# Kernel tuning notes

Measured on AMD Instinct MI355X. Metric: run time of the kernel, lower is better.

Reference implementation:

```python
import jax
import jax.numpy as jnp
from jax import lax
import numpy as np


def design_butter_hp_sos(order: int, cutoff: float, fs: float) -> np.ndarray:
    """Pure-numpy replica of scipy.signal.butter(order, cutoff, 'hp', fs=fs, output='sos')."""
    Wn = cutoff / (fs / 2.0)          # normalized to Nyquist
    fs_b = 2.0                        # scipy's internal sampling rate convention
    warped = 2.0 * fs_b * np.tan(np.pi * Wn / fs_b)  # prewarped analog cutoff
    # Analog Butterworth lowpass prototype poles (buttap)
    m = np.arange(-order + 1, order, 2)
    p_lp = -np.exp(1j * np.pi * m / (2 * order))
    k = np.real(np.prod(-p_lp))       # == 1 for Butterworth
    # lp2hp: zeros at s=0, poles -> warped / p
    p_hp = warped / p_lp
    z_hp = np.zeros(order, dtype=complex)
    # bilinear transform (fs2 = 2 * fs_b)
    fs2 = 2.0 * fs_b
    p_z = (fs2 + p_hp) / (fs2 - p_hp)
    k_z = k * np.real(np.prod(fs2 - z_hp) / np.prod(fs2 - p_hp))
    # pair conjugate poles into biquads; scipy puts poles nearest unit circle LAST
    pos = p_z[np.imag(p_z) > 0]
    pos = pos[np.argsort(np.abs(pos))]
    n_sec = order // 2
    sos = np.zeros((n_sec, 6))
    for i, p in enumerate(pos):
        b = np.array([1.0, -2.0, 1.0])  # two zeros at z = 1 (DC block)
        if i == 0:
            b = b * k_z                 # overall gain lives in the first section
        sos[i, :3] = b
        sos[i, 3:] = np.array([1.0, -2.0 * p.real, np.abs(p) ** 2])
    return sos.astype(np.float32)


def setup_inputs() -> dict:
    key = jax.random.key(0)
    audio = jax.random.normal(key, (64, 480000), dtype=jnp.float32)  # [batch, samples]
    sos = jnp.asarray(design_butter_hp_sos(4, 80.0, 16000.0))        # [2, 6]
    return {"audio": audio, "sos": sos}


def _sosfilt(sos, x):
    """Cascade biquad IIR (direct form II transposed), zero initial state.
    x: [B, T], sos: [n_sections, 6]. Batch is vectorized inside the scan carry."""
    B = x.shape[0]

    def one_section(x, coefs):
        b0, b1, b2, _, a1, a2 = coefs

        def step(state, xn):
            s0, s1 = state                 # each [B]
            y = b0 * xn + s0
            s0_new = b1 * xn - a1 * y + s1
            s1_new = b2 * xn - a2 * y
            return (s0_new, s1_new), y

        init = (jnp.zeros(B, x.dtype), jnp.zeros(B, x.dtype))
        _, y = lax.scan(step, init, x.T)   # scan over time, [T, B]
        return y.T

    for i in range(sos.shape[0]):          # small static loop over 2 sections
        x = one_section(x, sos[i])
    return x


def reference(audio, sos):
    squeeze = audio.ndim == 1
    x = audio[None, :] if squeeze else audio
    y = _sosfilt(sos, x)
    return y[0] if squeeze else y
```

## Files before the change

### kernel.cpp

```cpp
#include <hip/hip_runtime.h>


#define SEG   32
#define F4S   (SEG / 4)
#define NT    32
#define SEGS  256
#define EMITS (SEGS - NT)

typedef float f32x4 __attribute__((ext_vector_type(4)));

struct Coefs { float b00,b01,b02,a01,a02,b10,b11,b12,a11,a12; };

__device__ __forceinline__ void step(const Coefs& c, float xn,
    float& s10, float& s11, float& s20, float& s21, float& yout) {
  float y1 = fmaf(c.b00, xn, s10);
  s10 = fmaf(-c.a01, y1, fmaf(c.b01, xn, s11));
  s11 = fmaf(-c.a02, y1, c.b02 * xn);
  float y2 = fmaf(c.b10, y1, s20);
  s20 = fmaf(-c.a11, y2, fmaf(c.b11, y1, s21));
  s21 = fmaf(-c.a12, y2, c.b12 * y1);
  yout = y2;
}

__device__ __forceinline__ Coefs load_coefs(const float* __restrict__ sos) {
  Coefs c;
  c.b00=sos[0]; c.b01=sos[1]; c.b02=sos[2]; c.a01=sos[4];  c.a02=sos[5];
  c.b10=sos[6]; c.b11=sos[7]; c.b12=sos[8]; c.a11=sos[10]; c.a12=sos[11];
  return c;
}

__global__ __launch_bounds__(256, 4) void iir_fused(
    const float* __restrict__ x, const float* __restrict__ sos,
    float* __restrict__ out, int T, int nchunks, int bpr) {
  __shared__ f32x4 stg[SEGS * F4S];
  __shared__ f32x4 u[SEGS];

  int row = blockIdx.x / bpr;
  int blk = blockIdx.x - row * bpr;
  int k = threadIdx.x;
  int sbase = blk * EMITS - NT;
  int myseg = sbase + k;
  int perm = k & 7;
  Coefs c = load_coefs(sos);

  const f32x4* xr4 = reinterpret_cast<const f32x4*>(x) + (size_t)row * (T >> 2);
  f32x4*       yr4 = reinterpret_cast<f32x4*>(out)     + (size_t)row * (T >> 2);
  const f32x4 z4 = {0.f, 0.f, 0.f, 0.f};

  f32x4 t0,t1,t2,t3,t4,t5,t6,t7;
#define PREF(IT, TR) { int f_ = k + IT*256; int s_ = f_>>3; int gs_ = sbase + s_; \
    TR = (gs_ >= 0 && gs_ < nchunks) ? xr4[(size_t)gs_ * F4S + (f_&7)] : z4; }
#define WST(IT, TR) { int f_ = k + IT*256; int s_ = f_>>3, j_ = f_&7; \
    stg[s_*F4S + (j_^(s_&7))] = TR; }
  PREF(0,t0) PREF(1,t1) PREF(2,t2) PREF(3,t3)
  PREF(4,t4) PREF(5,t5) PREF(6,t6) PREF(7,t7)
  WST(0,t0) WST(1,t1) WST(2,t2) WST(3,t3)
  WST(4,t4) WST(5,t5) WST(6,t6) WST(7,t7)
  __syncthreads();

  {
    float s10 = 0.f, s11 = 0.f, s20 = 0.f, s21 = 0.f, d_;
#pragma unroll
    for (int j = 0; j < F4S; ++j) {
      f32x4 v = stg[k * F4S + (j ^ perm)];
      step(c, v[0], s10, s11, s20, s21, d_);
      step(c, v[1], s10, s11, s20, s21, d_);
      step(c, v[2], s10, s11, s20, s21, d_);
      step(c, v[3], s10, s11, s20, s21, d_);
    }
    f32x4 uu; uu[0] = s10; uu[1] = s11; uu[2] = s20; uu[3] = s21;
    u[k] = uu;
  }
  __syncthreads();

  float P[16];
  {
    float A[16];
#pragma unroll
    for (int col = 0; col < 4; ++col) {
      float a0 = (col == 0), a1 = (col == 1), a2 = (col == 2), a3 = (col == 3), dd;
      step(c, 0.f, a0, a1, a2, a3, dd);
      A[0 * 4 + col] = a0; A[1 * 4 + col] = a1;
      A[2 * 4 + col] = a2; A[3 * 4 + col] = a3;
    }
#pragma unroll
    for (int i = 0; i < 16; ++i) P[i] = A[i];
#pragma unroll
    for (int it = 0; it < 5; ++it) {
      float Q[16];
#pragma unroll
      for (int r = 0; r < 4; ++r)
#pragma unroll
        for (int cc = 0; cc < 4; ++cc) {
          float acc = 0.f;
#pragma unroll
          for (int kk = 0; kk < 4; ++kk) acc = fmaf(P[r * 4 + kk], P[kk * 4 + cc], acc);
          Q[r * 4 + cc] = acc;
        }
#pragma unroll
      for (int i = 0; i < 16; ++i) P[i] = Q[i];
    }
  }

  bool emits = (k >= NT) && (myseg < nchunks);
  if (emits) {
    float h0 = 0.f, h1 = 0.f, h2 = 0.f, h3 = 0.f;
#pragma unroll
    for (int kk = NT; kk >= 1; --kk) {
      f32x4 uu = u[k - kk];
      float q0 = fmaf(P[0],  h0, fmaf(P[1],  h1, fmaf(P[2],  h2, P[3]  * h3)));
      float q1 = fmaf(P[4],  h0, fmaf(P[5],  h1, fmaf(P[6],  h2, P[7]  * h3)));
      float q2 = fmaf(P[8],  h0, fmaf(P[9],  h1, fmaf(P[10], h2, P[11] * h3)));
      float q3 = fmaf(P[12], h0, fmaf(P[13], h1, fmaf(P[14], h2, P[15] * h3)));
      h0 = uu[0] + q0; h1 = uu[1] + q1; h2 = uu[2] + q2; h3 = uu[3] + q3;
    }
    float s10 = h0, s11 = h1, s20 = h2, s21 = h3;
#pragma unroll
    for (int j = 0; j < F4S; ++j) {
      f32x4 v = stg[k * F4S + (j ^ perm)];
      f32x4 yv; float yo;
      step(c, v[0], s10, s11, s20, s21, yo); yv[0] = yo;
      step(c, v[1], s10, s11, s20, s21, yo); yv[1] = yo;
      step(c, v[2], s10, s11, s20, s21, yo); yv[2] = yo;
      step(c, v[3], s10, s11, s20, s21, yo); yv[3] = yo;
      stg[k * F4S + (j ^ perm)] = yv;
    }
  }
  __syncthreads();

  int eseg0 = blk * EMITS;
  int nemit = nchunks - eseg0; if (nemit > EMITS) nemit = EMITS;
  if (nemit > 0) {
    int F = nemit * F4S;
    f32x4* dst = yr4 + (size_t)eseg0 * F4S;
    for (int f = k; f < F; f += 256) {
      int s = f >> 3, j = f & 7;
      int ls = s + NT;
      dst[f] = stg[ls * F4S + (j ^ (ls & 7))];
    }
  }
}

#define FB_C 256
#define FB_W 1024
__global__ __launch_bounds__(256) void sosfilt2_chunked(
    const float* __restrict__ x, const float* __restrict__ sos,
    float* __restrict__ out, int B, int T, int nchunks) {
  int tid = blockIdx.x * 256 + threadIdx.x;
  if (tid >= B * nchunks) return;
  int row = tid / nchunks;
  int chunk = tid - row * nchunks;
  Coefs c = load_coefs(sos);
  const float* xr = x + (size_t)row * T;
  float*       yr = out + (size_t)row * T;
  int c0   = chunk * FB_C;
  int cend = min(c0 + FB_C, T);
  int warm = min(FB_W, c0);
  int t    = c0 - warm;
  float s10 = 0.f, s11 = 0.f, s20 = 0.f, s21 = 0.f;
  float dump;
  for (; t < c0; t += 4) {
    f32x4 xvv = *reinterpret_cast<const f32x4*>(xr + t);
#pragma unroll
    for (int j = 0; j < 4; ++j) step(c, xvv[j], s10, s11, s20, s21, dump);
  }
  int tv_end = c0 + ((cend - c0) & ~3);
  for (; t < tv_end; t += 4) {
    f32x4 xvv = *reinterpret_cast<const f32x4*>(xr + t);
    f32x4 yv;
#pragma unroll
    for (int j = 0; j < 4; ++j) {
      float yo;
      step(c, xvv[j], s10, s11, s20, s21, yo);
      yv[j] = yo;
    }
    *reinterpret_cast<f32x4*>(yr + t) = yv;
  }
  for (; t < cend; ++t) { float yv; step(c, xr[t], s10, s11, s20, s21, yv); yr[t] = yv; }
}

extern "C" void kernel_launch(void* const* d_in, const int* in_sizes, int n_in,
                              void* d_out, int out_size, void* d_ws, size_t ws_size,
                              hipStream_t stream) {
  const float* x   = (const float*)d_in[0];
  const float* sos = (const float*)d_in[1];
  float*       out = (float*)d_out;

  int total = in_sizes[0];
  int T = 480000;
  if (total % T != 0) T = total;
  int B = total / T;

  if (T % SEG == 0) {
    int nchunks = T / SEG;
    int bpr = (nchunks + EMITS - 1) / EMITS;
    iir_fused<<<B * bpr, 256, 0, stream>>>(x, sos, out, T, nchunks, bpr);
  } else {
    int nc = (T + FB_C - 1) / FB_C;
    int grid = (B * nc + 255) / 256;
    sosfilt2_chunked<<<grid, 256, 0, stream>>>(x, sos, out, B, T, nc);
  }
}
```

Measured before the change: 50.18 us.

## Replace serial 32-step state propagation with log-depth parallel scan using precomputed matrix powers

```diff
diff --git a/kernel.cpp b/kernel.cpp
--- a/kernel.cpp
+++ b/kernel.cpp
@@ -29,11 +29,49 @@
   return c;
 }
 
+__global__ void iir_setup(const float* __restrict__ sos, float* __restrict__ ws) {
+  if (blockIdx.x != 0 || threadIdx.x != 0) return;
+  Coefs c = load_coefs(sos);
+  float P[16];
+  {
+    float A[16];
+    for (int col = 0; col < 4; ++col) {
+      float a0 = (col == 0), a1 = (col == 1), a2 = (col == 2), a3 = (col == 3), dd;
+      step(c, 0.f, a0, a1, a2, a3, dd);
+      A[0*4+col] = a0; A[1*4+col] = a1; A[2*4+col] = a2; A[3*4+col] = a3;
+    }
+    for (int i = 0; i < 16; ++i) P[i] = A[i];
+    for (int it = 0; it < 5; ++it) {
+      float Q[16];
+      for (int r = 0; r < 4; ++r)
+        for (int cc = 0; cc < 4; ++cc) {
+          float acc = 0.f;
+          for (int kk = 0; kk < 4; ++kk) acc = fmaf(P[r*4+kk], P[kk*4+cc], acc);
+          Q[r*4+cc] = acc;
+        }
+      for (int i = 0; i < 16; ++i) P[i] = Q[i];
+    }
+  }
+  for (int l = 0; l < 5; ++l) {
+    for (int i = 0; i < 16; ++i) ws[l*16 + i] = P[i];
+    float Q[16];
+    for (int r = 0; r < 4; ++r)
+      for (int cc = 0; cc < 4; ++cc) {
+        float acc = 0.f;
+        for (int kk = 0; kk < 4; ++kk) acc = fmaf(P[r*4+kk], P[kk*4+cc], acc);
+        Q[r*4+cc] = acc;
+      }
+    for (int i = 0; i < 16; ++i) P[i] = Q[i];
+  }
+}
+
 __global__ __launch_bounds__(256, 4) void iir_fused(
     const float* __restrict__ x, const float* __restrict__ sos,
-    float* __restrict__ out, int T, int nchunks, int bpr) {
+    const float* __restrict__ ws, float* __restrict__ out,
+    int T, int nchunks, int bpr) {
   __shared__ f32x4 stg[SEGS * F4S];
-  __shared__ f32x4 u[SEGS];
+  __shared__ f32x4 va[SEGS];
+  __shared__ f32x4 vb[SEGS];
 
   int row = blockIdx.x / bpr;
   int blk = blockIdx.x - row * bpr;
@@ -69,52 +107,48 @@
       step(c, v[3], s10, s11, s20, s21, d_);
     }
     f32x4 uu; uu[0] = s10; uu[1] = s11; uu[2] = s20; uu[3] = s21;
-    u[k] = uu;
-  }
-  __syncthreads();
-
-  float P[16];
-  {
-    float A[16];
-#pragma unroll
-    for (int col = 0; col < 4; ++col) {
-      float a0 = (col == 0), a1 = (col == 1), a2 = (col == 2), a3 = (col == 3), dd;
-      step(c, 0.f, a0, a1, a2, a3, dd);
-      A[0 * 4 + col] = a0; A[1 * 4 + col] = a1;
-      A[2 * 4 + col] = a2; A[3 * 4 + col] = a3;
-    }
-#pragma unroll
-    for (int i = 0; i < 16; ++i) P[i] = A[i];
-#pragma unroll
-    for (int it = 0; it < 5; ++it) {
-      float Q[16];
-#pragma unroll
-      for (int r = 0; r < 4; ++r)
-#pragma unroll
-        for (int cc = 0; cc < 4; ++cc) {
-          float acc = 0.f;
-#pragma unroll
-          for (int kk = 0; kk < 4; ++kk) acc = fmaf(P[r * 4 + kk], P[kk * 4 + cc], acc);
-          Q[r * 4 + cc] = acc;
-        }
-#pragma unroll
-      for (int i = 0; i < 16; ++i) P[i] = Q[i];
-    }
-  }
+    va[k] = uu;
+  }
+  __syncthreads();
+
+  {
+    f32x4 vprev = (k >= 1) ? va[k - 1] : z4;
+    __syncthreads();
+    va[k] = vprev;
+  }
+  __syncthreads();
+
+  {
+    f32x4* src = va;
+    f32x4* dst = vb;
+#pragma unroll
+    for (int l = 0; l < 5; ++l) {
+      float p0  = ws[l*16+0],  p1  = ws[l*16+1],  p2  = ws[l*16+2],  p3  = ws[l*16+3];
+      float p4  = ws[l*16+4],  p5  = ws[l*16+5],  p6  = ws[l*16+6],  p7  = ws[l*16+7];
+      float p8  = ws[l*16+8],  p9  = ws[l*16+9],  p10 = ws[l*16+10], p11 = ws[l*16+11];
+      float p12 = ws[l*16+12], p13 = ws[l*16+13], p14 = ws[l*16+14], p15 = ws[l*16+15];
+      f32x4 mine = src[k];
+      int off = 1 << l;
+      f32x4 r = mine;
+      if (k >= off) {
+        f32x4 w = src[k - off];
+        r[0] = mine[0] + fmaf(p0,  w[0], fmaf(p1,  w[1], fmaf(p2,  w[2], p3  * w[3])));
+        r[1] = mine[1] + fmaf(p4,  w[0], fmaf(p5,  w[1], fmaf(p6,  w[2], p7  * w[3])));
+        r[2] = mine[2] + fmaf(p8,  w[0], fmaf(p9,  w[1], fmaf(p10, w[2], p11 * w[3])));
+        r[3] = mine[3] + fmaf(p12, w[0], fmaf(p13, w[1], fmaf(p14, w[2], p15 * w[3])));
+      }
+      dst[k] = r;
+      __syncthreads();
+      f32x4* tmp = src; src = dst; dst = tmp;
+    }
+    va[k] = src[k];
+  }
+  __syncthreads();
 
   bool emits = (k >= NT) && (myseg < nchunks);
   if (emits) {
-    float h0 = 0.f, h1 = 0.f, h2 = 0.f, h3 = 0.f;
-#pragma unroll
-    for (int kk = NT; kk >= 1; --kk) {
-      f32x4 uu = u[k - kk];
-      float q0 = fmaf(P[0],  h0, fmaf(P[1],  h1, fmaf(P[2],  h2, P[3]  * h3)));
-      float q1 = fmaf(P[4],  h0, fmaf(P[5],  h1, fmaf(P[6],  h2, P[7]  * h3)));
-      float q2 = fmaf(P[8],  h0, fmaf(P[9],  h1, fmaf(P[10], h2, P[11] * h3)));
-      float q3 = fmaf(P[12], h0, fmaf(P[13], h1, fmaf(P[14], h2, P[15] * h3)));
-      h0 = uu[0] + q0; h1 = uu[1] + q1; h2 = uu[2] + q2; h3 = uu[3] + q3;
-    }
-    float s10 = h0, s11 = h1, s20 = h2, s21 = h3;
+    f32x4 s = va[k];
+    float s10 = s[0], s11 = s[1], s20 = s[2], s21 = s[3];
 #pragma unroll
     for (int j = 0; j < F4S; ++j) {
       f32x4 v = stg[k * F4S + (j ^ perm)];
@@ -191,10 +225,12 @@
   if (total % T != 0) T = total;
   int B = total / T;
 
-  if (T % SEG == 0) {
+  if (T % SEG == 0 && ws_size >= 80 * sizeof(float)) {
+    float* ws = (float*)d_ws;
     int nchunks = T / SEG;
     int bpr = (nchunks + EMITS - 1) / EMITS;
-    iir_fused<<<B * bpr, 256, 0, stream>>>(x, sos, out, T, nchunks, bpr);
+    iir_setup<<<1, 64, 0, stream>>>(sos, ws);
+    iir_fused<<<B * bpr, 256, 0, stream>>>(x, sos, ws, out, T, nchunks, bpr);
   } else {
     int nc = (T + FB_C - 1) / FB_C;
     int grid = (B * nc + 255) / 256;
```

Result: slower. 52.17 us (+4.0%).
